# Performance work log

Measured on AMD Instinct MI355X. Metric: run time of the kernel, lower is better.

## Reference

```python
import jax, jax.numpy as jnp
import numpy as np
from jax import lax

B, N, D, L, EDGE_H, NGNN = 8, 128, 256, 64, 64, 3


def setup_inputs() -> dict:
    key = jax.random.key(0)
    ks = iter(jax.random.split(key, 64))
    def nrm(shape, s=0.02):
        return jax.random.normal(next(ks), shape, jnp.float32) * s
    inp = {}
    inp["node_feats"] = jax.random.uniform(next(ks), (B, N, 11), jnp.float32)
    inp["edge_feats"] = jax.random.normal(next(ks), (B, N, N, 3), jnp.float32)
    inp["adj_mask"] = jax.random.randint(next(ks), (B, N, N), 0, 2).astype(bool)
    inp["layer_costs"] = jax.random.uniform(next(ks), (B, L), jnp.float32)
    inp["global_dynamic"] = jax.random.uniform(next(ks), (B, 2), jnp.float32)
    inp["p_node_w"] = nrm((11, D)); inp["p_node_b"] = jnp.zeros((D,), jnp.float32)
    inp["g_w1"] = nrm((NGNN, D + 3, EDGE_H)); inp["g_b1"] = jnp.zeros((NGNN, EDGE_H), jnp.float32)
    inp["g_w2"] = nrm((NGNN, EDGE_H, D)); inp["g_b2"] = jnp.zeros((NGNN, D), jnp.float32)
    inp["u_w1"] = nrm((NGNN, 3 * D, D)); inp["u_b1"] = jnp.zeros((NGNN, D), jnp.float32)
    inp["u_w2"] = nrm((NGNN, D, D)); inp["u_b2"] = jnp.zeros((NGNN, D), jnp.float32)
    inp["ln_g"] = jnp.ones((NGNN, D), jnp.float32); inp["ln_b"] = jnp.zeros((NGNN, D), jnp.float32)
    inp["conv_w"] = nrm((32, 1, 4)); inp["conv_b"] = jnp.zeros((32,), jnp.float32)
    inp["lp_w"] = nrm((32 * 31, D)); inp["lp_b"] = jnp.zeros((D,), jnp.float32)
    inp["q_w"] = nrm((2 * D + 2, D)); inp["q_b"] = jnp.zeros((D,), jnp.float32)
    inp["k_w"] = nrm((D, D)); inp["k_b"] = jnp.zeros((D,), jnp.float32)
    inp["s_w1"] = nrm((D + 2, D)); inp["s_b1"] = jnp.zeros((D,), jnp.float32)
    inp["s_w2"] = nrm((D, 1)); inp["s_b2"] = jnp.zeros((1,), jnp.float32)
    inp["v_w1"] = nrm((2 * D + 2, D)); inp["v_b1"] = jnp.zeros((D,), jnp.float32)
    inp["v_w2"] = nrm((D, 1)); inp["v_b2"] = jnp.zeros((1,), jnp.float32)
    return inp


def _ecgc(h, edge_feats, adj_bool, gw1, gb1, gw2, gb2, uw1, ub1, uw2, ub2, lng, lnb):
    Bh, Nn, Dd = h.shape
    # h_j: features of sender node j broadcast over receiver axis -> (B, N, N, D)
    h_j = jnp.broadcast_to(h[:, None, :, :], (Bh, Nn, Nn, Dd))
    gate_in = jnp.concatenate([h_j, edge_feats], axis=-1)            # (B,N,N,D+3)
    gates = jax.nn.sigmoid(jax.nn.relu(gate_in @ gw1 + gb1) @ gw2 + gb2)
    msg = gates * h_j                                                # (B,N,N,D)
    m = adj_bool.astype(h.dtype)[..., None]
    cnt = jnp.maximum(m.sum(axis=2), 1.0)                            # (B,N,1)
    agg_mean = (msg * m).sum(axis=2) / cnt                           # (B,N,D)
    agg_max = jnp.where(adj_bool[..., None], msg, -jnp.inf).max(axis=2)
    agg_max = jnp.where(jnp.isinf(agg_max), 0.0, agg_max)
    ui = jnp.concatenate([h, agg_mean, agg_max], axis=-1)            # (B,N,3D)
    x = h + (jax.nn.relu(ui @ uw1 + ub1) @ uw2 + ub2)
    mu = x.mean(-1, keepdims=True)
    var = ((x - mu) ** 2).mean(-1, keepdims=True)
    return (x - mu) * lax.rsqrt(var + 1e-5) * lng + lnb


def reference(node_feats, edge_feats, adj_mask, layer_costs, global_dynamic,
              p_node_w, p_node_b, g_w1, g_b1, g_w2, g_b2, u_w1, u_b1, u_w2, u_b2,
              ln_g, ln_b, conv_w, conv_b, lp_w, lp_b, q_w, q_b, k_w, k_b,
              s_w1, s_b1, s_w2, s_b2, v_w1, v_b1, v_w2, v_b2):
    # layer cost encoder: Conv1d(1,32,k=4,s=2) + ReLU, flatten, Linear
    le = lax.conv_general_dilated(layer_costs[:, None, :], conv_w, (2,), 'VALID',
                                  dimension_numbers=('NCH', 'OIH', 'NCH'))
    le = jax.nn.relu(le + conv_b[None, :, None])                     # (B,32,31)
    layer_embed = le.reshape(le.shape[0], -1) @ lp_w + lp_b          # (B,D)
    h = node_feats @ p_node_w + p_node_b                             # (B,N,D)
    for i in range(g_w1.shape[0]):
        h = _ecgc(h, edge_feats, adj_mask, g_w1[i], g_b1[i], g_w2[i], g_b2[i],
                  u_w1[i], u_b1[i], u_w2[i], u_b2[i], ln_g[i], ln_b[i])
    w = (node_feats[:, :, 0] * node_feats[:, :, 7])[..., None]       # (B,N,1)
    graph_embed = (w * h).sum(axis=1) / jnp.maximum(w.sum(axis=1), 1e-8)
    qi = jnp.concatenate([graph_embed, layer_embed, global_dynamic], axis=-1)
    query = qi @ q_w + q_b                                           # (B,D)
    keys = h @ k_w + k_b                                             # (B,N,D)
    device_scores = jnp.einsum('bnd,bd->bn', keys, query) / jnp.sqrt(jnp.float32(query.shape[-1]))
    si = jnp.concatenate([graph_embed, global_dynamic], axis=-1)
    stop_logit = jax.nn.relu(si @ s_w1 + s_b1) @ s_w2 + s_b2         # (B,1)
    all_logits = jnp.concatenate([device_scores, stop_logit], axis=1)
    value = jax.nn.relu(qi @ v_w1 + v_b1) @ v_w2 + v_b2              # (B,1)
    return all_logits, value, h
```

## Files before the change

### kernel.cpp

```cpp
#include <hip/hip_runtime.h>
#include <hip/hip_bf16.h>
#include <math.h>

#define BB 8
#define NN_ 128
#define DD 256
#define LL 64
#define EH 64
#define NG 3

typedef __attribute__((ext_vector_type(8))) short bs8;
typedef __attribute__((ext_vector_type(4))) float f4;

__device__ __forceinline__ short f2bf(float f) {
    __hip_bfloat16 h = __float2bfloat16(f);
    return *reinterpret_cast<short*>(&h);
}

__device__ __forceinline__ bs8 cvt8(const float* __restrict__ p) {
    bs8 r;
    #pragma unroll
    for (int i = 0; i < 8; ++i) r[i] = f2bf(p[i]);
    return r;
}

__device__ __forceinline__ float blockReduceSum(float v, float* sRed) {
    int tid = threadIdx.x;
    __syncthreads();
    sRed[tid] = v;
    __syncthreads();
    for (int s = 128; s > 0; s >>= 1) {
        if (tid < s) sRed[tid] += sRed[tid + s];
        __syncthreads();
    }
    return sRed[0];
}

__global__ __launch_bounds__(256) void k_prep(
    const float* __restrict__ uw1, const float* __restrict__ uw2,
    const float* __restrict__ gw2, const float* __restrict__ gw1,
    const float* __restrict__ kw, const unsigned char* __restrict__ adj,
    unsigned short* __restrict__ w1t, unsigned short* __restrict__ w2t,
    unsigned short* __restrict__ g2t, unsigned short* __restrict__ g1t,
    unsigned short* __restrict__ kwt, int* __restrict__ mode)
{
    const int blk = blockIdx.x, tid = threadIdx.x;
    if (blk == 232) {
        __shared__ int sOff, sBig;
        if (tid == 0) { sOff = 0; sBig = 0; }
        __syncthreads();
        int off = 0, big = 0;
        #pragma unroll
        for (int k = 0; k < 4; ++k) {
            unsigned char v = adj[tid * 4 + k];
            if (v > 1) big = 1;
            if (k != 0 && v != 0) off = 1;
        }
        if (off) atomicOr(&sOff, 1);
        if (big) atomicOr(&sBig, 1);
        __syncthreads();
        if (tid == 0) mode[0] = sBig ? 2 : (sOff ? 0 : 1);
        return;
    }
    const float* src; unsigned short* dst; int K, kt, dt, srcw = 256;
    if (blk < 144)      { int l = blk / 48, t = blk % 48; kt = t >> 2; dt = t & 3;
                          src = uw1 + (size_t)l * 196608; dst = w1t + (size_t)l * 196608; K = 768; }
    else if (blk < 192) { int x = blk - 144, l = x / 16, t = x % 16; kt = t >> 2; dt = t & 3;
                          src = uw2 + (size_t)l * 65536; dst = w2t + (size_t)l * 65536; K = 256; }
    else if (blk < 204) { int x = blk - 192, l = x >> 2; kt = 0; dt = x & 3;
                          src = gw2 + (size_t)l * 16384; dst = g2t + (size_t)l * 16384; K = 64; }
    else if (blk < 216) { int x = blk - 204, l = x >> 2; kt = x & 3; dt = 0; srcw = 64;
                          src = gw1 + (size_t)l * 16576; dst = g1t + (size_t)l * 16384; K = 256; }
    else                { int x = blk - 216; kt = x >> 2; dt = x & 3;
                          src = kw; dst = kwt; K = 256; }
    __shared__ float sT[64][65];
    #pragma unroll
    for (int q = 0; q < 16; ++q) {
        int idx = q * 256 + tid, kk = idx >> 6, dd = idx & 63;
        sT[kk][dd] = src[(size_t)(kt * 64 + kk) * srcw + dt * 64 + dd];
    }
    __syncthreads();
    const int d = tid >> 2, kc = (tid & 3) * 16;
    unsigned short* drow = dst + (size_t)(dt * 64 + d) * K + kt * 64 + kc;
    #pragma unroll
    for (int i = 0; i < 16; ++i) drow[i] = (unsigned short)f2bf(sT[kc + i][d]);
}

__global__ __launch_bounds__(256) void k_nodeproj(
    const float* __restrict__ nf, const float* __restrict__ w,
    const float* __restrict__ bias, float* __restrict__ h)
{
    const int row = blockIdx.x, tid = threadIdx.x;
    __shared__ float sF[11];
    if (tid < 11) sF[tid] = nf[(size_t)row * 11 + tid];
    __syncthreads();
    float a = bias[tid];
    #pragma unroll
    for (int f = 0; f < 11; ++f) a += sF[f] * w[f * DD + tid];
    h[(size_t)row * DD + tid] = a;
}

__global__ __launch_bounds__(256) void k_lmm(
    const float* __restrict__ lc, const float* __restrict__ cw,
    const float* __restrict__ cb, const float* __restrict__ lpw,
    float* __restrict__ part)
{
    const int blk = blockIdx.x;
    const int b = blk >> 5, kseg = (blk >> 2) & 7, c4 = blk & 3;
    const int tid = threadIdx.x;
    const int d = tid & 63, ss = tid >> 6;
    __shared__ float sC[LL];
    __shared__ float sV[124];
    __shared__ float sP[4][64];
    if (tid < LL) sC[tid] = lc[b * LL + tid];
    __syncthreads();
    if (tid < 124) {
        int idx = kseg * 124 + tid;
        int c = idx / 31, t = idx - c * 31;
        float a = cb[c];
        #pragma unroll
        for (int k = 0; k < 4; ++k) a += sC[2 * t + k] * cw[c * 4 + k];
        sV[tid] = fmaxf(a, 0.f);
    }
    __syncthreads();
    float acc = 0.f;
    for (int k = ss; k < 124; k += 4)
        acc += sV[k] * lpw[(size_t)(kseg * 124 + k) * DD + c4 * 64 + d];
    sP[ss][d] = acc;
    __syncthreads();
    if (ss == 0)
        part[(b * 32 + kseg * 4 + c4) * 64 + d] = sP[0][d] + sP[1][d] + sP[2][d] + sP[3][d];
}

__global__ __launch_bounds__(256) void k_pregate(
    const float* __restrict__ h, const unsigned short* __restrict__ g1t,
    const float* __restrict__ gb1, float* __restrict__ preg)
{
    const int tid = threadIdx.x, blk = blockIdx.x;
    const int row0 = blk * 16;
    const int lane = tid & 63, w = tid >> 6;
    const int lcol = lane & 15, lrow = lane >> 4;
    const float* aR = h + (size_t)(row0 + lcol) * DD;
    const unsigned short* bR = g1t + (size_t)(w * 16 + lcol) * 256;
    f4 acc = {0.f, 0.f, 0.f, 0.f};
    #pragma unroll
    for (int ks = 0; ks < 8; ++ks) {
        int k0 = ks * 32 + lrow * 8;
        bs8 av = cvt8(aR + k0);
        bs8 bv = *(const bs8*)(bR + k0);
        acc = __builtin_amdgcn_mfma_f32_16x16x32_bf16(av, bv, acc, 0, 0, 0);
    }
    const float gb = gb1[w * 16 + lcol];
    #pragma unroll
    for (int r = 0; r < 4; ++r)
        preg[(size_t)(row0 + lrow * 4 + r) * EH + w * 16 + lcol] = acc[r] + gb;
}

__global__ __launch_bounds__(256) void k_edge(
    const float* __restrict__ h, const float* __restrict__ preg,
    const float* __restrict__ edge, const void* __restrict__ adj,
    const int* __restrict__ mode,
    const float* __restrict__ gw1,
    const unsigned short* __restrict__ g2t,
    const float* __restrict__ gb2,
    float* __restrict__ agg_mean, float* __restrict__ agg_max)
{
    const int tid = threadIdx.x;
    const int bi = blockIdx.x;
    const int b = bi >> 7;
    const int lane = tid & 63, w = tid >> 6;
    const int lrow = lane >> 4, lcol = lane & 15;
    const int md = mode[0];

    __shared__ __align__(16) unsigned int sHid[4096];
    __shared__ float sWe[192];
    __shared__ float sE[384];
    __shared__ unsigned long long sMask[2];

    if (tid < 192) sWe[tid] = gw1[16384 + tid];
    const float* eB = edge + (size_t)bi * 384;
    for (int idx = tid; idx < 384; idx += 256) sE[idx] = eB[idx];
    if (tid < 128) {
        int mv;
        if (md == 1)      mv = ((const int*)adj)[(size_t)bi * NN_ + tid] != 0;
        else if (md == 2) mv = ((const float*)adj)[(size_t)bi * NN_ + tid] != 0.f;
        else              mv = ((const unsigned char*)adj)[(size_t)bi * NN_ + tid] != 0;
        unsigned long long bal = __ballot(mv);
        if ((tid & 63) == 0) sMask[tid >> 6] = bal;
    }
    __syncthreads();

    const float* pB = preg + (size_t)b * NN_ * EH;
    #pragma unroll
    for (int q = 0; q < 16; ++q) {
        int idx = q * 256 + tid;
        int j = idx >> 5, p = idx & 31;
        float2 pv = *(const float2*)(pB + j * EH + 2 * p);
        float e0 = sE[j * 3], e1 = sE[j * 3 + 1], e2 = sE[j * 3 + 2];
        int t0 = 2 * p, t1 = t0 + 1;
        float v0 = fmaxf(pv.x + e0 * sWe[t0] + e1 * sWe[64 + t0] + e2 * sWe[128 + t0], 0.f);
        float v1 = fmaxf(pv.y + e0 * sWe[t1] + e1 * sWe[64 + t1] + e2 * sWe[128 + t1], 0.f);
        unsigned int pk = (unsigned int)(unsigned short)f2bf(v0) |
                          ((unsigned int)(unsigned short)f2bf(v1) << 16);
        sHid[j * 32 + (p ^ ((j & 7) << 2))] = pk;
    }
    __syncthreads();

    const unsigned long long m0 = sMask[0], m1 = sMask[1];
    const float cntf = (float)(__popcll(m0) + __popcll(m1));

    bs8 bfr[4][2];
    float bg[4];
    #pragma unroll
    for (int nt = 0; nt < 4; ++nt) {
        int d = w * 64 + nt * 16 + lcol;
        bg[nt] = gb2[d];
        #pragma unroll
        for (int ks = 0; ks < 2; ++ks) {
            int k0 = ks * 32 + lrow * 8;
            bfr[nt][ks] = *(const bs8*)(g2t + (size_t)d * 64 + k0);
        }
    }

    const float* hB = h + (size_t)b * NN_ * DD;
    float vs[4] = {0.f, 0.f, 0.f, 0.f};
    float vm[4] = {-INFINITY, -INFINITY, -INFINITY, -INFINITY};

    #pragma unroll
    for (int pp = 0; pp < 2; ++pp) {
        f4 acc[4][4] = {};
        #pragma unroll
        for (int ks = 0; ks < 2; ++ks) {
            bs8 afr[4];
            #pragma unroll
            for (int m = 0; m < 4; ++m) {
                int j = pp * 64 + m * 16 + lcol;
                int k0 = ks * 32 + lrow * 8;
                afr[m] = *(const bs8*)(sHid + (j * 32 + ((k0 >> 1) ^ ((j & 7) << 2))));
            }
            #pragma unroll
            for (int m = 0; m < 4; ++m)
                #pragma unroll
                for (int nt = 0; nt < 4; ++nt)
                    acc[m][nt] = __builtin_amdgcn_mfma_f32_16x16x32_bf16(
                        afr[m], bfr[nt][ks], acc[m][nt], 0, 0, 0);
        }
        const unsigned long long mw = pp ? m1 : m0;
        #pragma unroll
        for (int m = 0; m < 4; ++m) {
            #pragma unroll
            for (int nt = 0; nt < 4; ++nt) {
                int dnt = w * 64 + nt * 16 + lcol;
                #pragma unroll
                for (int r = 0; r < 4; ++r) {
                    int bit = m * 16 + lrow * 4 + r;
                    float x = acc[m][nt][r] + bg[nt];
                    float g = __builtin_amdgcn_rcpf(1.0f + __expf(-x));
                    float msg = g * hB[(pp * 64 + bit) * DD + dnt];
                    int on = (int)((mw >> bit) & 1ULL);
                    vs[nt] += on ? msg : 0.f;
                    vm[nt] = fmaxf(vm[nt], on ? msg : -INFINITY);
                }
            }
        }
    }

    #pragma unroll
    for (int nt = 0; nt < 4; ++nt) {
        float s = vs[nt];
        s += __shfl_xor(s, 16); s += __shfl_xor(s, 32);
        vs[nt] = s;
        float m = vm[nt];
        m = fmaxf(m, __shfl_xor(m, 16)); m = fmaxf(m, __shfl_xor(m, 32));
        vm[nt] = m;
    }
    const int g = lrow;
    float ssel = (g == 0) ? vs[0] : (g == 1) ? vs[1] : (g == 2) ? vs[2] : vs[3];
    float msel = (g == 0) ? vm[0] : (g == 1) ? vm[1] : (g == 2) ? vm[2] : vm[3];
    const int d = w * 64 + lane;
    agg_mean[(size_t)bi * DD + d] = ssel / fmaxf(cntf, 1.f);
    agg_max[(size_t)bi * DD + d] = (cntf > 0.f) ? msel : 0.f;
}

__global__ __launch_bounds__(256) void k_upd(
    const float* __restrict__ h, const float* __restrict__ amean,
    const float* __restrict__ amax,
    const unsigned short* __restrict__ w1t,
    const float* __restrict__ ub1,
    const unsigned short* __restrict__ w2t,
    const float* __restrict__ ub2,
    const float* __restrict__ lng, const float* __restrict__ lnb,
    float* __restrict__ hout, float* __restrict__ out2)
{
    const int tid = threadIdx.x;
    const int row0 = blockIdx.x * 4;
    const int lane = tid & 63, w = tid >> 6;
    const int lcol = lane & 15, lrow = lane >> 4;

    __shared__ __align__(16) unsigned int sX32[16 * 384];
    __shared__ __align__(16) unsigned short sH16[16 * 256];
    __shared__ float sRes[4][256];
    __shared__ float sOut[4][256];

    {
        const int j = w;
        const float* hR = h + (size_t)(row0 + j) * DD;
        const float* mR = amean + (size_t)(row0 + j) * DD;
        const float* xR = amax + (size_t)(row0 + j) * DD;
        #pragma unroll
        for (int q = 0; q < 6; ++q) {
            int p = lane + q * 64;
            int k = 2 * p;
            float2 v;
            if (k < 256)      { v = *(const float2*)(hR + k); sRes[j][k] = v.x; sRes[j][k + 1] = v.y; }
            else if (k < 512)   v = *(const float2*)(mR + (k - 256));
            else                v = *(const float2*)(xR + (k - 512));
            unsigned int pk = (unsigned int)(unsigned short)f2bf(v.x) |
                              ((unsigned int)(unsigned short)f2bf(v.y) << 16);
            sX32[j * 384 + (p ^ (j << 2))] = pk;
        }
    }
    __syncthreads();

    const char* sXb = (const char*)sX32;
    const unsigned short* w1r = w1t + (size_t)(w * 64 + lcol) * 768;
    f4 a0 = {0.f, 0.f, 0.f, 0.f}, a1 = a0, a2 = a0, a3 = a0;
    #pragma unroll 4
    for (int ks = 0; ks < 24; ++ks) {
        int k0 = ks * 32 + lrow * 8;
        bs8 av = *(const bs8*)(sXb + lcol * 1536 + ((((k0 >> 3) ^ (lcol & 7))) << 4));
        bs8 b0 = *(const bs8*)(w1r + k0);
        bs8 b1 = *(const bs8*)(w1r + 16 * 768 + k0);
        bs8 b2 = *(const bs8*)(w1r + 32 * 768 + k0);
        bs8 b3 = *(const bs8*)(w1r + 48 * 768 + k0);
        a0 = __builtin_amdgcn_mfma_f32_16x16x32_bf16(av, b0, a0, 0, 0, 0);
        a1 = __builtin_amdgcn_mfma_f32_16x16x32_bf16(av, b1, a1, 0, 0, 0);
        a2 = __builtin_amdgcn_mfma_f32_16x16x32_bf16(av, b2, a2, 0, 0, 0);
        a3 = __builtin_amdgcn_mfma_f32_16x16x32_bf16(av, b3, a3, 0, 0, 0);
    }
    if (lrow == 0) {
        #pragma unroll
        for (int nt = 0; nt < 4; ++nt) {
            int d = w * 64 + nt * 16 + lcol;
            float bb = ub1[d];
            f4 A = (nt == 0) ? a0 : (nt == 1) ? a1 : (nt == 2) ? a2 : a3;
            #pragma unroll
            for (int r = 0; r < 4; ++r) {
                float hv = fmaxf(A[r] + bb, 0.f);
                sH16[r * 256 + (d ^ (r << 3))] = (unsigned short)f2bf(hv);
            }
        }
    }
    __syncthreads();

    const unsigned short* w2r = w2t + (size_t)(w * 64 + lcol) * 256;
    f4 c0 = {0.f, 0.f, 0.f, 0.f}, c1 = c0, c2 = c0, c3 = c0;
    #pragma unroll
    for (int ks = 0; ks < 8; ++ks) {
        int k0 = ks * 32 + lrow * 8;
        bs8 av = *(const bs8*)((const char*)sH16 + lcol * 512 + ((((k0 >> 3) ^ (lcol & 7))) << 4));
        bs8 b0 = *(const bs8*)(w2r + k0);
        bs8 b1 = *(const bs8*)(w2r + 16 * 256 + k0);
        bs8 b2 = *(const bs8*)(w2r + 32 * 256 + k0);
        bs8 b3 = *(const bs8*)(w2r + 48 * 256 + k0);
        c0 = __builtin_amdgcn_mfma_f32_16x16x32_bf16(av, b0, c0, 0, 0, 0);
        c1 = __builtin_amdgcn_mfma_f32_16x16x32_bf16(av, b1, c1, 0, 0, 0);
        c2 = __builtin_amdgcn_mfma_f32_16x16x32_bf16(av, b2, c2, 0, 0, 0);
        c3 = __builtin_amdgcn_mfma_f32_16x16x32_bf16(av, b3, c3, 0, 0, 0);
    }
    if (lrow == 0) {
        #pragma unroll
        for (int nt = 0; nt < 4; ++nt) {
            int d = w * 64 + nt * 16 + lcol;
            float bb = ub2[d];
            f4 C = (nt == 0) ? c0 : (nt == 1) ? c1 : (nt == 2) ? c2 : c3;
            #pragma unroll
            for (int r = 0; r < 4; ++r)
                sOut[r][d] = C[r] + bb + sRes[r][d];
        }
    }
    __syncthreads();

    float xv[4], s = 0.f;
    #pragma unroll
    for (int q = 0; q < 4; ++q) { xv[q] = sOut[w][lane + 64 * q]; s += xv[q]; }
    #pragma unroll
    for (int off = 1; off < 64; off <<= 1) s += __shfl_xor(s, off);
    const float mu = s * (1.f / DD);
    float s2 = 0.f;
    #pragma unroll
    for (int q = 0; q < 4; ++q) { float d = xv[q] - mu; s2 += d * d; }
    #pragma unroll
    for (int off = 1; off < 64; off <<= 1) s2 += __shfl_xor(s2, off);
    const float inv = rsqrtf(s2 * (1.f / DD) + 1e-5f);
    #pragma unroll
    for (int q = 0; q < 4; ++q) {
        int c = lane + 64 * q;
        float res = (xv[q] - mu) * inv * lng[c] + lnb[c];
        hout[(size_t)(row0 + w) * DD + c] = res;
        if (out2) out2[(size_t)(row0 + w) * DD + c] = res;
    }
}

__global__ __launch_bounds__(256) void k_gembed(
    const float* __restrict__ nf, const float* __restrict__ h, float* __restrict__ ge)
{
    const int b = blockIdx.x, tid = threadIdx.x;
    __shared__ float sW[NN_];
    __shared__ float sRed[256];
    if (tid < NN_) {
        const float* p = nf + ((size_t)b * NN_ + tid) * 11;
        sW[tid] = p[0] * p[7];
    }
    __syncthreads();
    float part = (tid < NN_) ? sW[tid] : 0.f;
    float wsum = blockReduceSum(part, sRed);
    const float* hb = h + (size_t)b * NN_ * DD + tid;
    float a0 = 0.f, a1 = 0.f, a2 = 0.f, a3 = 0.f;
    for (int n = 0; n < 32; ++n) {
        a0 += sW[n]      * hb[(size_t)n * DD];
        a1 += sW[n + 32] * hb[(size_t)(n + 32) * DD];
        a2 += sW[n + 64] * hb[(size_t)(n + 64) * DD];
        a3 += sW[n + 96] * hb[(size_t)(n + 96) * DD];
    }
    ge[b * DD + tid] = (a0 + a1 + a2 + a3) / fmaxf(wsum, 1e-8f);
}

__global__ __launch_bounds__(256) void k_hmm(
    const float* __restrict__ ge, const float* __restrict__ gd,
    const float* __restrict__ qw, const float* __restrict__ sw1,
    const float* __restrict__ vw1,
    const float* __restrict__ lpb, const float* __restrict__ lpart,
    float* __restrict__ part)
{
    const int blk = blockIdx.x;
    const int m = blk >> 5, kseg = (blk >> 2) & 7, c4 = blk & 3;
    const int tid = threadIdx.x;
    const int d = tid & 63, ks = tid >> 6;
    const int K = (m == 1) ? 258 : 514;
    const int kc = (m == 1) ? 33 : 65;
    const int k0 = kseg * kc;
    const int klen = min(k0 + kc, K) - k0;
    __shared__ float sX[8 * 66];
    __shared__ float sP[4][8][64];
    for (int idx = tid; idx < 8 * kc; idx += 256) {
        int bb = idx / kc, kk = idx % kc, k = k0 + kk;
        float v = 0.f;
        if (k < K) {
            if (m == 1) v = (k < 256) ? ge[bb * DD + k] : gd[bb * 2 + (k - 256)];
            else if (k < 256) v = ge[bb * DD + k];
            else if (k < 512) {
                int e = k - 256;
                v = lpb[e];
                #pragma unroll
                for (int s = 0; s < 8; ++s)
                    v += lpart[(bb * 32 + s * 4 + (e >> 6)) * 64 + (e & 63)];
            } else v = gd[bb * 2 + (k - 512)];
        }
        sX[bb * 66 + kk] = v;
    }
    __syncthreads();
    const float* W = (m == 0) ? qw : (m == 1) ? sw1 : vw1;
    const int dg = c4 * 64 + d;
    float acc[8] = {0.f, 0.f, 0.f, 0.f, 0.f, 0.f, 0.f, 0.f};
    for (int kk = ks; kk < klen; kk += 4) {
        float wv = W[(size_t)(k0 + kk) * DD + dg];
        #pragma unroll
        for (int bb = 0; bb < 8; ++bb) acc[bb] += sX[bb * 66 + kk] * wv;
    }
    #pragma unroll
    for (int bb = 0; bb < 8; ++bb) sP[ks][bb][d] = acc[bb];
    __syncthreads();
    for (int idx = tid; idx < 8 * 64; idx += 256) {
        int bb = idx >> 6, dd = idx & 63;
        float sum = sP[0][bb][dd] + sP[1][bb][dd] + sP[2][bb][dd] + sP[3][bb][dd];
        part[((m * 8 + kseg) * 8 + bb) * DD + c4 * 64 + dd] = sum;
    }
}

__global__ __launch_bounds__(256) void k_hfin(
    const float* __restrict__ part,
    const float* __restrict__ qb, const float* __restrict__ sb1,
    const float* __restrict__ vb1,
    const float* __restrict__ sw2, const float* __restrict__ sb2,
    const float* __restrict__ vw2, const float* __restrict__ vb2,
    float* __restrict__ query, float* __restrict__ out)
{
    const int b = blockIdx.x, tid = threadIdx.x;
    __shared__ float sRed[256];
    float q = qb[tid], s = sb1[tid], v = vb1[tid];
    #pragma unroll
    for (int kseg = 0; kseg < 8; ++kseg) {
        q += part[((0 * 8 + kseg) * 8 + b) * DD + tid];
        s += part[((1 * 8 + kseg) * 8 + b) * DD + tid];
        v += part[((2 * 8 + kseg) * 8 + b) * DD + tid];
    }
    query[b * DD + tid] = q;
    s = fmaxf(s, 0.f); v = fmaxf(v, 0.f);
    float stop = blockReduceSum(s * sw2[tid], sRed);
    float val  = blockReduceSum(v * vw2[tid], sRed);
    if (tid == 0) {
        out[b * 129 + 128] = stop + sb2[0];
        out[1032 + b] = val + vb2[0];
    }
}

__global__ __launch_bounds__(256) void k_scores(
    const float* __restrict__ h, const unsigned short* __restrict__ kwt,
    const float* __restrict__ kb, const float* __restrict__ query,
    float* __restrict__ out)
{
    const int tid = threadIdx.x, blk = blockIdx.x;
    const int row0 = blk * 16, b = blk >> 3;
    const int lane = tid & 63, w = tid >> 6;
    const int lcol = lane & 15, lrow = lane >> 4;
    __shared__ float sPart[4][16];
    const float* aR = h + (size_t)(row0 + lcol) * DD;
    f4 acc[4] = {};
    #pragma unroll
    for (int ks = 0; ks < 8; ++ks) {
        int k0 = ks * 32 + lrow * 8;
        bs8 av = cvt8(aR + k0);
        #pragma unroll
        for (int nt = 0; nt < 4; ++nt) {
            bs8 bv = *(const bs8*)(kwt + (size_t)(w * 64 + nt * 16 + lcol) * 256 + k0);
            acc[nt] = __builtin_amdgcn_mfma_f32_16x16x32_bf16(av, bv, acc[nt], 0, 0, 0);
        }
    }
    float part[4] = {0.f, 0.f, 0.f, 0.f};
    #pragma unroll
    for (int nt = 0; nt < 4; ++nt) {
        int col = w * 64 + nt * 16 + lcol;
        float q = query[b * DD + col], kv = kb[col];
        #pragma unroll
        for (int r = 0; r < 4; ++r) part[r] += (acc[nt][r] + kv) * q;
    }
    #pragma unroll
    for (int r = 0; r < 4; ++r) {
        float s = part[r];
        s += __shfl_xor(s, 1); s += __shfl_xor(s, 2);
        s += __shfl_xor(s, 4); s += __shfl_xor(s, 8);
        part[r] = s;
    }
    if (lcol == 0) {
        #pragma unroll
        for (int r = 0; r < 4; ++r) sPart[w][lrow * 4 + r] = part[r];
    }
    __syncthreads();
    if (tid < 16) {
        float s = sPart[0][tid] + sPart[1][tid] + sPart[2][tid] + sPart[3][tid];
        out[b * 129 + (row0 & (NN_ - 1)) + tid] = s * 0.0625f;
    }
}

extern "C" void kernel_launch(void* const* d_in, const int* in_sizes, int n_in,
                              void* d_out, int out_size, void* d_ws, size_t ws_size,
                              hipStream_t stream) {
    (void)in_sizes; (void)n_in; (void)out_size; (void)ws_size;
    const float* nf  = (const float*)d_in[0];
    const float* ef  = (const float*)d_in[1];
    const void*  adj = d_in[2];
    const float* lc  = (const float*)d_in[3];
    const float* gd  = (const float*)d_in[4];
    const float* pnw = (const float*)d_in[5];
    const float* pnb = (const float*)d_in[6];
    const float* gw1 = (const float*)d_in[7];
    const float* gb1 = (const float*)d_in[8];
    const float* gw2 = (const float*)d_in[9];
    const float* gb2 = (const float*)d_in[10];
    const float* uw1 = (const float*)d_in[11];
    const float* ub1 = (const float*)d_in[12];
    const float* uw2 = (const float*)d_in[13];
    const float* ub2 = (const float*)d_in[14];
    const float* lng = (const float*)d_in[15];
    const float* lnb = (const float*)d_in[16];
    const float* cw  = (const float*)d_in[17];
    const float* cb  = (const float*)d_in[18];
    const float* lpw = (const float*)d_in[19];
    const float* lpb = (const float*)d_in[20];
    const float* qw  = (const float*)d_in[21];
    const float* qb  = (const float*)d_in[22];
    const float* kw  = (const float*)d_in[23];
    const float* kb  = (const float*)d_in[24];
    const float* sw1 = (const float*)d_in[25];
    const float* sb1 = (const float*)d_in[26];
    const float* sw2 = (const float*)d_in[27];
    const float* sb2 = (const float*)d_in[28];
    const float* vw1 = (const float*)d_in[29];
    const float* vb1 = (const float*)d_in[30];
    const float* vw2 = (const float*)d_in[31];
    const float* vb2 = (const float*)d_in[32];

    float* ws = (float*)d_ws;
    float* h     = ws;
    float* preg  = ws + 262144;
    float* amean = ws + 327680;
    float* amax  = ws + 589824;
    float* ge    = ws + 851968;
    float* query = ws + 854016;
    float* lpart = ws + 856064;
    float* hpart = ws + 872448;
    int*   mode  = (int*)(ws + 921600);
    unsigned short* uw1t = (unsigned short*)(ws + 921604);
    unsigned short* uw2t = (unsigned short*)(ws + 1216516);
    unsigned short* g2t  = (unsigned short*)(ws + 1314820);
    unsigned short* g1t  = (unsigned short*)(ws + 1339396);
    unsigned short* kwt  = (unsigned short*)(ws + 1363972);
    float* out   = (float*)d_out;

    k_prep<<<233, 256, 0, stream>>>(uw1, uw2, gw2, gw1, kw,
                                    (const unsigned char*)adj,
                                    uw1t, uw2t, g2t, g1t, kwt, mode);
    k_nodeproj<<<BB * NN_, 256, 0, stream>>>(nf, pnw, pnb, h);
    k_lmm<<<256, 256, 0, stream>>>(lc, cw, cb, lpw, lpart);
    k_pregate<<<BB * NN_ / 16, 256, 0, stream>>>(h, g1t, gb1, preg);
    for (int i = 0; i < NG; ++i) {
        const float* gw1i = gw1 + (size_t)i * 259 * EH;
        float* out2sel = (i == NG - 1) ? (out + 1040) : (float*)nullptr;
        k_edge<<<BB * NN_, 256, 0, stream>>>(h, preg, ef, adj, mode, gw1i,
                                             g2t + (size_t)i * 16384,
                                             gb2 + i * DD, amean, amax);
        k_upd<<<BB * NN_ / 4, 256, 0, stream>>>(h, amean, amax,
                                                uw1t + (size_t)i * 196608, ub1 + i * DD,
                                                uw2t + (size_t)i * 65536, ub2 + i * DD,
                                                lng + i * DD, lnb + i * DD, h, out2sel);
        if (i < NG - 1)
            k_pregate<<<BB * NN_ / 16, 256, 0, stream>>>(h, g1t + (size_t)(i + 1) * 16384,
                                                         gb1 + (i + 1) * EH, preg);
    }
    k_gembed<<<BB, 256, 0, stream>>>(nf, h, ge);
    k_hmm<<<96, 256, 0, stream>>>(ge, gd, qw, sw1, vw1, lpb, lpart, hpart);
    k_hfin<<<BB, 256, 0, stream>>>(hpart, qb, sb1, vb1, sw2, sb2, vw2, vb2, query, out);
    k_scores<<<BB * NN_ / 16, 256, 0, stream>>>(h, kwt, kb, query, out);
}
```

Measured before the change: 198.8 us.

## Fuse small kernels to cut launch count across prep, pregate, update and scoring

Folds the layer-embedding conv+matmul into the weight-prep kernel as extra blocks. Merges node projection with the first pregate matmul, and fuses each subsequent pregate into the tail of the update kernel using the freshly normalized rows kept in shared memory. Merges the head finalization into the scores kernel, so each block recomputes the query in shared memory. This removes about six launches and some global round-trips, at the cost of extra per-block work and a bf16 MFMA that uses only 4 of its 16 rows in the update tail.

```diff
diff --git a/kernel.cpp b/kernel.cpp
--- a/kernel.cpp
+++ b/kernel.cpp
@@ -40,9 +40,12 @@
     const float* __restrict__ uw1, const float* __restrict__ uw2,
     const float* __restrict__ gw2, const float* __restrict__ gw1,
     const float* __restrict__ kw, const unsigned char* __restrict__ adj,
+    const float* __restrict__ lc, const float* __restrict__ cw,
+    const float* __restrict__ cb, const float* __restrict__ lpw,
     unsigned short* __restrict__ w1t, unsigned short* __restrict__ w2t,
     unsigned short* __restrict__ g2t, unsigned short* __restrict__ g1t,
-    unsigned short* __restrict__ kwt, int* __restrict__ mode)
+    unsigned short* __restrict__ kwt, int* __restrict__ mode,
+    float* __restrict__ lpart)
 {
     const int blk = blockIdx.x, tid = threadIdx.x;
     if (blk == 232) {
@@ -60,6 +63,33 @@
         if (big) atomicOr(&sBig, 1);
         __syncthreads();
         if (tid == 0) mode[0] = sBig ? 2 : (sOff ? 0 : 1);
+        return;
+    }
+    if (blk > 232) {
+        const int lb = blk - 233;
+        const int b = lb >> 5, kseg = (lb >> 2) & 7, c4 = lb & 3;
+        const int d = tid & 63, ss = tid >> 6;
+        __shared__ float sC[LL];
+        __shared__ float sV[124];
+        __shared__ float sP[4][64];
+        if (tid < LL) sC[tid] = lc[b * LL + tid];
+        __syncthreads();
+        if (tid < 124) {
+            int idx = kseg * 124 + tid;
+            int c = idx / 31, t = idx - c * 31;
+            float a = cb[c];
+            #pragma unroll
+            for (int k = 0; k < 4; ++k) a += sC[2 * t + k] * cw[c * 4 + k];
+            sV[tid] = fmaxf(a, 0.f);
+        }
+        __syncthreads();
+        float acc = 0.f;
+        for (int k = ss; k < 124; k += 4)
+            acc += sV[k] * lpw[(size_t)(kseg * 124 + k) * DD + c4 * 64 + d];
+        sP[ss][d] = acc;
+        __syncthreads();
+        if (ss == 0)
+            lpart[(b * 32 + kseg * 4 + c4) * 64 + d] = sP[0][d] + sP[1][d] + sP[2][d] + sP[3][d];
         return;
     }
     const float* src; unsigned short* dst; int K, kt, dt, srcw = 256;
@@ -86,74 +116,51 @@
     for (int i = 0; i < 16; ++i) drow[i] = (unsigned short)f2bf(sT[kc + i][d]);
 }
 
-__global__ __launch_bounds__(256) void k_nodeproj(
-    const float* __restrict__ nf, const float* __restrict__ w,
-    const float* __restrict__ bias, float* __restrict__ h)
-{
-    const int row = blockIdx.x, tid = threadIdx.x;
-    __shared__ float sF[11];
-    if (tid < 11) sF[tid] = nf[(size_t)row * 11 + tid];
-    __syncthreads();
-    float a = bias[tid];
-    #pragma unroll
-    for (int f = 0; f < 11; ++f) a += sF[f] * w[f * DD + tid];
-    h[(size_t)row * DD + tid] = a;
-}
-
-__global__ __launch_bounds__(256) void k_lmm(
-    const float* __restrict__ lc, const float* __restrict__ cw,
-    const float* __restrict__ cb, const float* __restrict__ lpw,
-    float* __restrict__ part)
-{
-    const int blk = blockIdx.x;
-    const int b = blk >> 5, kseg = (blk >> 2) & 7, c4 = blk & 3;
-    const int tid = threadIdx.x;
-    const int d = tid & 63, ss = tid >> 6;
-    __shared__ float sC[LL];
-    __shared__ float sV[124];
-    __shared__ float sP[4][64];
-    if (tid < LL) sC[tid] = lc[b * LL + tid];
-    __syncthreads();
-    if (tid < 124) {
-        int idx = kseg * 124 + tid;
-        int c = idx / 31, t = idx - c * 31;
-        float a = cb[c];
-        #pragma unroll
-        for (int k = 0; k < 4; ++k) a += sC[2 * t + k] * cw[c * 4 + k];
-        sV[tid] = fmaxf(a, 0.f);
-    }
-    __syncthreads();
-    float acc = 0.f;
-    for (int k = ss; k < 124; k += 4)
-        acc += sV[k] * lpw[(size_t)(kseg * 124 + k) * DD + c4 * 64 + d];
-    sP[ss][d] = acc;
-    __syncthreads();
-    if (ss == 0)
-        part[(b * 32 + kseg * 4 + c4) * 64 + d] = sP[0][d] + sP[1][d] + sP[2][d] + sP[3][d];
-}
-
-__global__ __launch_bounds__(256) void k_pregate(
-    const float* __restrict__ h, const unsigned short* __restrict__ g1t,
-    const float* __restrict__ gb1, float* __restrict__ preg)
+__global__ __launch_bounds__(256) void k_npp(
+    const float* __restrict__ nf, const float* __restrict__ pnw,
+    const float* __restrict__ pnb,
+    const unsigned short* __restrict__ g1t, const float* __restrict__ gb1,
+    float* __restrict__ h, float* __restrict__ preg)
 {
     const int tid = threadIdx.x, blk = blockIdx.x;
     const int row0 = blk * 16;
     const int lane = tid & 63, w = tid >> 6;
     const int lcol = lane & 15, lrow = lane >> 4;
-    const float* aR = h + (size_t)(row0 + lcol) * DD;
+    __shared__ float sF[16][12];
+    __shared__ float sH[16][260];
+    if (tid < 176) sF[tid / 11][tid % 11] = nf[(size_t)(row0 + tid / 11) * 11 + tid % 11];
+    __syncthreads();
+    float acc[16];
+    {
+        float bb = pnb[tid];
+        #pragma unroll
+        for (int rr = 0; rr < 16; ++rr) acc[rr] = bb;
+    }
+    #pragma unroll
+    for (int f = 0; f < 11; ++f) {
+        float wf = pnw[f * DD + tid];
+        #pragma unroll
+        for (int rr = 0; rr < 16; ++rr) acc[rr] += sF[rr][f] * wf;
+    }
+    #pragma unroll
+    for (int rr = 0; rr < 16; ++rr) {
+        sH[rr][tid] = acc[rr];
+        h[(size_t)(row0 + rr) * DD + tid] = acc[rr];
+    }
+    __syncthreads();
     const unsigned short* bR = g1t + (size_t)(w * 16 + lcol) * 256;
-    f4 acc = {0.f, 0.f, 0.f, 0.f};
+    f4 a2 = {0.f, 0.f, 0.f, 0.f};
     #pragma unroll
     for (int ks = 0; ks < 8; ++ks) {
         int k0 = ks * 32 + lrow * 8;
-        bs8 av = cvt8(aR + k0);
+        bs8 av = cvt8(&sH[lcol][k0]);
         bs8 bv = *(const bs8*)(bR + k0);
-        acc = __builtin_amdgcn_mfma_f32_16x16x32_bf16(av, bv, acc, 0, 0, 0);
+        a2 = __builtin_amdgcn_mfma_f32_16x16x32_bf16(av, bv, a2, 0, 0, 0);
     }
     const float gb = gb1[w * 16 + lcol];
     #pragma unroll
     for (int r = 0; r < 4; ++r)
-        preg[(size_t)(row0 + lrow * 4 + r) * EH + w * 16 + lcol] = acc[r] + gb;
+        preg[(size_t)(row0 + lrow * 4 + r) * EH + w * 16 + lcol] = a2[r] + gb;
 }
 
 __global__ __launch_bounds__(256) void k_edge(
@@ -282,7 +289,7 @@
     agg_max[(size_t)bi * DD + d] = (cntf > 0.f) ? msel : 0.f;
 }
 
-__global__ __launch_bounds__(256) void k_upd(
+__global__ __launch_bounds__(256) void k_updp(
     const float* __restrict__ h, const float* __restrict__ amean,
     const float* __restrict__ amax,
     const unsigned short* __restrict__ w1t,
@@ -290,7 +297,9 @@
     const unsigned short* __restrict__ w2t,
     const float* __restrict__ ub2,
     const float* __restrict__ lng, const float* __restrict__ lnb,
-    float* __restrict__ hout, float* __restrict__ out2)
+    float* __restrict__ hout, float* __restrict__ out2,
+    const unsigned short* __restrict__ g1tn, const float* __restrict__ gb1n,
+    float* __restrict__ preg)
 {
     const int tid = threadIdx.x;
     const int row0 = blockIdx.x * 4;
@@ -300,7 +309,7 @@
     __shared__ __align__(16) unsigned int sX32[16 * 384];
     __shared__ __align__(16) unsigned short sH16[16 * 256];
     __shared__ float sRes[4][256];
-    __shared__ float sOut[4][256];
+    __shared__ float sOut[4][260];
 
     {
         const int j = w;
@@ -399,6 +408,25 @@
         float res = (xv[q] - mu) * inv * lng[c] + lnb[c];
         hout[(size_t)(row0 + w) * DD + c] = res;
         if (out2) out2[(size_t)(row0 + w) * DD + c] = res;
+        sOut[w][c] = res;
+    }
+    if (g1tn) {
+        __syncthreads();
+        const unsigned short* bR = g1tn + (size_t)(w * 16 + lcol) * 256;
+        f4 p = {0.f, 0.f, 0.f, 0.f};
+        #pragma unroll
+        for (int ks = 0; ks < 8; ++ks) {
+            int k0 = ks * 32 + lrow * 8;
+            bs8 av = cvt8(&sOut[lcol & 3][k0]);
+            bs8 bv = *(const bs8*)(bR + k0);
+            p = __builtin_amdgcn_mfma_f32_16x16x32_bf16(av, bv, p, 0, 0, 0);
+        }
+        if (lrow == 0) {
+            const float gb = gb1n[w * 16 + lcol];
+            #pragma unroll
+            for (int r = 0; r < 4; ++r)
+                preg[(size_t)(row0 + r) * EH + w * 16 + lcol] = p[r] + gb;
+        }
     }
 }
 
@@ -478,43 +506,30 @@
     }
 }
 
-__global__ __launch_bounds__(256) void k_hfin(
-    const float* __restrict__ part,
-    const float* __restrict__ qb, const float* __restrict__ sb1,
-    const float* __restrict__ vb1,
+__global__ __launch_bounds__(256) void k_scr(
+    const float* __restrict__ h, const unsigned short* __restrict__ kwt,
+    const float* __restrict__ kb, const float* __restrict__ hpart,
+    const float* __restrict__ qb,
+    const float* __restrict__ sb1, const float* __restrict__ vb1,
     const float* __restrict__ sw2, const float* __restrict__ sb2,
     const float* __restrict__ vw2, const float* __restrict__ vb2,
-    float* __restrict__ query, float* __restrict__ out)
-{
-    const int b = blockIdx.x, tid = threadIdx.x;
-    __shared__ float sRed[256];
-    float q = qb[tid], s = sb1[tid], v = vb1[tid];
-    #pragma unroll
-    for (int kseg = 0; kseg < 8; ++kseg) {
-        q += part[((0 * 8 + kseg) * 8 + b) * DD + tid];
-        s += part[((1 * 8 + kseg) * 8 + b) * DD + tid];
-        v += part[((2 * 8 + kseg) * 8 + b) * DD + tid];
-    }
-    query[b * DD + tid] = q;
-    s = fmaxf(s, 0.f); v = fmaxf(v, 0.f);
-    float stop = blockReduceSum(s * sw2[tid], sRed);
-    float val  = blockReduceSum(v * vw2[tid], sRed);
-    if (tid == 0) {
-        out[b * 129 + 128] = stop + sb2[0];
-        out[1032 + b] = val + vb2[0];
-    }
-}
-
-__global__ __launch_bounds__(256) void k_scores(
-    const float* __restrict__ h, const unsigned short* __restrict__ kwt,
-    const float* __restrict__ kb, const float* __restrict__ query,
     float* __restrict__ out)
 {
     const int tid = threadIdx.x, blk = blockIdx.x;
-    const int row0 = blk * 16, b = blk >> 3;
+    const int row0 = blk * 16, b = blk >> 3, chunk = blk & 7;
     const int lane = tid & 63, w = tid >> 6;
     const int lcol = lane & 15, lrow = lane >> 4;
+    __shared__ float sQ[256];
     __shared__ float sPart[4][16];
+    __shared__ float sRed[256];
+    {
+        float qv = qb[tid];
+        #pragma unroll
+        for (int kseg = 0; kseg < 8; ++kseg)
+            qv += hpart[(size_t)(kseg * 8 + b) * DD + tid];
+        sQ[tid] = qv;
+    }
+    __syncthreads();
     const float* aR = h + (size_t)(row0 + lcol) * DD;
     f4 acc[4] = {};
     #pragma unroll
@@ -531,7 +546,7 @@
     #pragma unroll
     for (int nt = 0; nt < 4; ++nt) {
         int col = w * 64 + nt * 16 + lcol;
-        float q = query[b * DD + col], kv = kb[col];
+        float q = sQ[col], kv = kb[col];
         #pragma unroll
         for (int r = 0; r < 4; ++r) part[r] += (acc[nt][r] + kv) * q;
     }
@@ -550,6 +565,21 @@
     if (tid < 16) {
         float s = sPart[0][tid] + sPart[1][tid] + sPart[2][tid] + sPart[3][tid];
         out[b * 129 + (row0 & (NN_ - 1)) + tid] = s * 0.0625f;
+    }
+    if (chunk == 0) {
+        float s = sb1[tid], v = vb1[tid];
+        #pragma unroll
+        for (int kseg = 0; kseg < 8; ++kseg) {
+            s += hpart[(size_t)((8 + kseg) * 8 + b) * DD + tid];
+            v += hpart[(size_t)((16 + kseg) * 8 + b) * DD + tid];
+        }
+        s = fmaxf(s, 0.f); v = fmaxf(v, 0.f);
+        float stop = blockReduceSum(s * sw2[tid], sRed);
+        float val  = blockReduceSum(v * vw2[tid], sRed);
+        if (tid == 0) {
+            out[b * 129 + 128] = stop + sb2[0];
+            out[1032 + b] = val + vb2[0];
+        }
     }
 }
 
@@ -597,7 +627,6 @@
     float* amean = ws + 327680;
     float* amax  = ws + 589824;
     float* ge    = ws + 851968;
-    float* query = ws + 854016;
     float* lpart = ws + 856064;
     float* hpart = ws + 872448;
     int*   mode  = (int*)(ws + 921600);
@@ -608,28 +637,28 @@
     unsigned short* kwt  = (unsigned short*)(ws + 1363972);
     float* out   = (float*)d_out;
 
-    k_prep<<<233, 256, 0, stream>>>(uw1, uw2, gw2, gw1, kw,
+    k_prep<<<489, 256, 0, stream>>>(uw1, uw2, gw2, gw1, kw,
                                     (const unsigned char*)adj,
-                                    uw1t, uw2t, g2t, g1t, kwt, mode);
-    k_nodeproj<<<BB * NN_, 256, 0, stream>>>(nf, pnw, pnb, h);
-    k_lmm<<<256, 256, 0, stream>>>(lc, cw, cb, lpw, lpart);
-    k_pregate<<<BB * NN_ / 16, 256, 0, stream>>>(h, g1t, gb1, preg);
+                                    lc, cw, cb, lpw,
+                                    uw1t, uw2t, g2t, g1t, kwt, mode, lpart);
+    k_npp<<<BB * NN_ / 16, 256, 0, stream>>>(nf, pnw, pnb, g1t, gb1, h, preg);
     for (int i = 0; i < NG; ++i) {
         const float* gw1i = gw1 + (size_t)i * 259 * EH;
         float* out2sel = (i == NG - 1) ? (out + 1040) : (float*)nullptr;
+        const unsigned short* g1tn = (i < NG - 1) ? (g1t + (size_t)(i + 1) * 16384)
+                                                  : (const unsigned short*)nullptr;
+        const float* gb1n = (i < NG - 1) ? (gb1 + (i + 1) * EH) : (const float*)nullptr;
         k_edge<<<BB * NN_, 256, 0, stream>>>(h, preg, ef, adj, mode, gw1i,
                                              g2t + (size_t)i * 16384,
                                              gb2 + i * DD, amean, amax);
-        k_upd<<<BB * NN_ / 4, 256, 0, stream>>>(h, amean, amax,
-                                                uw1t + (size_t)i * 196608, ub1 + i * DD,
-                                                uw2t + (size_t)i * 65536, ub2 + i * DD,
-                                                lng + i * DD, lnb + i * DD, h, out2sel);
-        if (i < NG - 1)
-            k_pregate<<<BB * NN_ / 16, 256, 0, stream>>>(h, g1t + (size_t)(i + 1) * 16384,
-                                                         gb1 + (i + 1) * EH, preg);
+        k_updp<<<BB * NN_ / 4, 256, 0, stream>>>(h, amean, amax,
+                                                 uw1t + (size_t)i * 196608, ub1 + i * DD,
+                                                 uw2t + (size_t)i * 65536, ub2 + i * DD,
+                                                 lng + i * DD, lnb + i * DD, h, out2sel,
+                                                 g1tn, gb1n, preg);
     }
     k_gembed<<<BB, 256, 0, stream>>>(nf, h, ge);
     k_hmm<<<96, 256, 0, stream>>>(ge, gd, qw, sw1, vw1, lpb, lpart, hpart);
-    k_hfin<<<BB, 256, 0, stream>>>(hpart, qb, sb1, vb1, sw2, sb2, vw2, vb2, query, out);
-    k_scores<<<BB * NN_ / 16, 256, 0, stream>>>(h, kwt, kb, query, out);
-}
+    k_scr<<<BB * NN_ / 16, 256, 0, stream>>>(h, kwt, kb, hpart, qb, sb1, vb1,
+                                             sw2, sb2, vw2, vb2, out);
+}
```

Result: faster. 183.9 us (median of 2 runs) (-7.5%).
